# Optimization experiments

Hardware: AMD Instinct MI355X
Metric: run time of the kernel (lower is better)

## Reference

```python
import jax, jax.numpy as jnp
import numpy as np

B, T, D, H = 4, 4096, 256, 64  # batch, seq, DIM_EMBEDDING (fixed constant), head_size


def setup_inputs() -> dict:
    key = jax.random.key(0)
    ks = jax.random.split(key, 6)
    x = jax.random.normal(ks[0], (B, T, D), dtype=jnp.float32)
    scale = jnp.float32(0.02)
    Wq = jax.random.normal(ks[1], (D, H), dtype=jnp.float32) * scale
    Wk = jax.random.normal(ks[2], (D, H), dtype=jnp.float32) * scale
    Wv = jax.random.normal(ks[3], (D, H), dtype=jnp.float32) * scale
    two_pi = jnp.float32(2.0 * np.pi)
    angles_x = jax.random.uniform(ks[4], (T, H // 4), dtype=jnp.float32, maxval=two_pi)
    angles_y = jax.random.uniform(ks[5], (T, H // 4), dtype=jnp.float32, maxval=two_pi)
    return {"x": x, "Wq": Wq, "Wk": Wk, "Wv": Wv, "angles_x": angles_x, "angles_y": angles_y}


def _rope_half(v, freqs):
    # v: (B, T, H/2) real; freqs: (T, H/4) complex64 (unit phasors)
    b, t, h = v.shape
    vc = v.astype(jnp.float32).reshape(b, t, h // 2, 2)
    vz = jax.lax.complex(vc[..., 0], vc[..., 1])         # (B, T, H/4)
    rz = vz * freqs[None]                                 # complex multiply per position
    out = jnp.stack([jnp.real(rz), jnp.imag(rz)], axis=-1)
    return out.reshape(b, t, h)


def _rope2d(v, fx, fy):
    vx, vy = jnp.split(v, 2, axis=-1)
    return jnp.concatenate([_rope_half(vx, fx), _rope_half(vy, fy)], axis=-1)


def reference(x, Wq, Wk, Wv, angles_x, angles_y):
    # complex unit phasors e^{i*theta}
    fx = jax.lax.complex(jnp.cos(angles_x), jnp.sin(angles_x))
    fy = jax.lax.complex(jnp.cos(angles_y), jnp.sin(angles_y))
    # original apply_rotary_embeddings is wrapped in @torch.no_grad -> detached
    q = jax.lax.stop_gradient(_rope2d(x @ Wq, fx, fy))
    k = jax.lax.stop_gradient(_rope2d(x @ Wk, fx, fy))
    v = x @ Wv
    C = x.shape[-1]  # NOTE: source scales by embedding dim (256), not head dim
    wei = jnp.einsum('bth,bsh->bts', q, k) / jnp.sqrt(jnp.float32(C))
    softwei = jax.nn.softmax(wei, axis=-1)  # no causal mask in source
    out = jnp.einsum('bts,bsh->bth', softwei, v)
    return out
```

## Files before the change

### kernel.cpp

```cpp
#include <hip/hip_runtime.h>

#define B_ 4
#define T_ 4096
#define D_ 256
#define H_ 64
#define NBT (B_ * T_)
#define NBTH (B_ * T_ * H_)

typedef __bf16 bf16x8 __attribute__((ext_vector_type(8)));
typedef float f32x4 __attribute__((ext_vector_type(4)));

__device__ __forceinline__ unsigned short f2bf(float f) {
  union { float f; unsigned int u; } v; v.f = f;
  unsigned int u = v.u;
  return (unsigned short)((u + 0x7fffu + ((u >> 16) & 1u)) >> 16);
}

#if __has_builtin(__builtin_amdgcn_cvt_pk_bf16_f32)
typedef __bf16 bf16x2_t __attribute__((ext_vector_type(2)));
__device__ __forceinline__ unsigned int pk2(float a, float b) {
  union { bf16x2_t v; unsigned int u; } c;
  c.v = __builtin_amdgcn_cvt_pk_bf16_f32(a, b);
  return c.u;
}
#else
__device__ __forceinline__ unsigned int pk2(float a, float b) {
  return (unsigned int)f2bf(a) | ((unsigned int)f2bf(b) << 16);
}
#endif

#if __has_builtin(__builtin_amdgcn_exp2f)
#define EXP2(x) __builtin_amdgcn_exp2f(x)
#else
#define EXP2(x) exp2f(x)
#endif

#define QSCALE 0.09016844f


__global__ __launch_bounds__(256) void prep_w_kernel(
    const float* __restrict__ Wq, const float* __restrict__ Wk,
    const float* __restrict__ Wv, unsigned short* __restrict__ wt) {
  const int m = blockIdx.x;
  const float* W = (m == 0) ? Wq : (m == 1) ? Wk : Wv;
  const float scale = (m == 0) ? QSCALE : 1.f;
  __shared__ unsigned short tile[64][264];
  int h = threadIdx.x & 63, dq = threadIdx.x >> 6;
  for (int d = dq; d < D_; d += 4)
    tile[h][d] = f2bf(W[d * H_ + h] * scale);
  __syncthreads();
  int ht = threadIdx.x >> 6;
  int lane = threadIdx.x & 63, quad = lane >> 4, l16 = lane & 15;
#pragma unroll
  for (int c = 0; c < 8; ++c) {
    bf16x8 v = *(const bf16x8*)&tile[ht * 16 + l16][c * 32 + quad * 8];
    *(bf16x8*)&wt[(((m * 4 + ht) * 8 + c) << 9) + lane * 8] = v;
  }
}

__global__ __launch_bounds__(192) void qkv_kernel(
    const float* __restrict__ x, const unsigned short* __restrict__ wt,
    const float* __restrict__ axg, const float* __restrict__ ayg,
    unsigned short* __restrict__ qo, unsigned short* __restrict__ ko,
    unsigned short* __restrict__ vt) {
  const int row0g = blockIdx.x * 16;
  const int tid = threadIdx.x;
  const int w = tid / 64, lane = tid & 63, quad = lane >> 4, l16 = lane & 15;

  __shared__ unsigned short xs[16][264];
  __shared__ unsigned short qkt[2][16][72];
  __shared__ unsigned short vsh[64][16];

  const float4* xb = (const float4*)(x + (size_t)row0g * D_);
  for (int i = tid; i < 1024; i += 192) {
    float4 v = xb[i];
    int r = i >> 6, c4 = (i & 63) << 2;
    *(unsigned int*)&xs[r][c4] = pk2(v.x, v.y);
    *(unsigned int*)&xs[r][c4 + 2] = pk2(v.z, v.w);
  }
  __syncthreads();

  bf16x8 xf[8];
#pragma unroll
  for (int c = 0; c < 8; ++c)
    xf[c] = *(const bf16x8*)&xs[l16][c * 32 + quad * 8];

  const unsigned short* wb = wt + (((size_t)w * 4) * 8 << 9);
  f32x4 acc[4];
#pragma unroll
  for (int ht = 0; ht < 4; ++ht) acc[ht] = (f32x4){0.f, 0.f, 0.f, 0.f};
#pragma unroll
  for (int c = 0; c < 8; ++c) {
#pragma unroll
    for (int ht = 0; ht < 4; ++ht) {
      bf16x8 wf = *(const bf16x8*)&wb[((ht * 8 + c) << 9) + lane * 8];
      acc[ht] = __builtin_amdgcn_mfma_f32_16x16x32_bf16(xf[c], wf, acc[ht],
                                                        0, 0, 0);
    }
  }

  const int row0loc = row0g & (T_ - 1);
  if (w < 2) {
    const float sgn = (l16 & 1) ? 1.f : -1.f;
#pragma unroll
    for (int ht = 0; ht < 4; ++ht) {
      int hh = ht * 16 + l16;
      int pidx = (hh & 31) >> 1;
      const float* ab = (hh >= 32) ? ayg : axg;
#pragma unroll
      for (int r = 0; r < 4; ++r) {
        int t = row0loc + quad * 4 + r;
        float s, c;
        __sincosf(ab[t * 16 + pidx], &s, &c);
        float val = acc[ht][r];
        float par = __shfl_xor(val, 1);
        qkt[w][quad * 4 + r][hh] = f2bf(val * c + sgn * par * s);
      }
    }
    asm volatile("s_waitcnt lgkmcnt(0)" ::: "memory");
    unsigned short* dst;
    size_t base;
    if (w == 0) {
      dst = qo;
      base = ((size_t)(row0g >> 4) * 2) << 9;
    } else {
      dst = ko;
      base = ((size_t)((row0g >> 6) * 8 + ((row0g >> 4) & 3) * 2)) << 9;
    }
#pragma unroll
    for (int half = 0; half < 2; ++half) {
      bf16x8 v = *(const bf16x8*)&qkt[w][l16][half * 32 + quad * 8];
      *(bf16x8*)&dst[base + half * 512 + lane * 8] = v;
    }
  } else {
#pragma unroll
    for (int ht = 0; ht < 4; ++ht)
#pragma unroll
      for (int r = 0; r < 4; ++r)
        vsh[ht * 16 + l16][quad * 4 + r] = f2bf(acc[ht][r]);
    asm volatile("s_waitcnt lgkmcnt(0)" ::: "memory");
    const int kvblk = row0g >> 6;
    const int mt = (row0g >> 4) & 3;
    const int half_v = mt >> 1, qlow = (mt & 1) * 2;
#pragma unroll
    for (int it = 0; it < 2; ++it) {
      int hhx = it * 2 + (quad >> 1);
      int qp = qlow + (quad & 1);
      bf16x8 v = *(const bf16x8*)&vsh[hhx * 16 + l16][(quad & 1) * 8];
      *(bf16x8*)&vt[((((size_t)kvblk * 4 + hhx) * 2 + half_v) << 9) +
                    (qp * 16 + l16) * 8] = v;
    }
  }
}

#define LDP 72

__global__ __launch_bounds__(256, 3) void attn_kernel(
    const unsigned short* __restrict__ qfg, const unsigned short* __restrict__ kfg,
    const unsigned short* __restrict__ vfg, float* __restrict__ opart,
    float* __restrict__ lpart, int kv_len) {
  const int split = blockIdx.x >> 7;
  const int rem = blockIdx.x & 127;
  const int b = rem >> 5;
  const int q0 = (rem & 31) * 128;
  const int tid = threadIdx.x;
  const int w = tid >> 6, lane = tid & 63, quad = lane >> 4, l16 = lane & 15;

  __shared__ unsigned short Ps[4][32 * LDP];

  bf16x8 ones;
  {
    union { bf16x8 v; unsigned int u[4]; } c;
    c.u[0] = c.u[1] = c.u[2] = c.u[3] = 0x3F803F80u;
    ones = c.v;
  }

  bf16x8 qf[2][2];
#pragma unroll
  for (int u = 0; u < 2; ++u) {
    size_t rb = (size_t)(b * T_ + q0 + w * 32 + u * 16) >> 4;
#pragma unroll
    for (int half = 0; half < 2; ++half)
      qf[u][half] = *(const bf16x8*)&qfg[((rb * 2 + half) << 9) + lane * 8];
  }

  f32x4 oacc[2][4], lacc[2];
  const f32x4 vzero = {0.f, 0.f, 0.f, 0.f};
#pragma unroll
  for (int u = 0; u < 2; ++u) {
    lacc[u] = vzero;
#pragma unroll
    for (int hh = 0; hh < 4; ++hh) oacc[u][hh] = vzero;
  }

  const int kvb0 = (b * T_ + split * kv_len) >> 6;
  const int nkvb = kv_len >> 6;

  for (int kb = 0; kb < nkvb; ++kb) {
    const unsigned short* kfb = kfg + ((size_t)(kvb0 + kb) << 12);
    const unsigned short* vfb = vfg + ((size_t)(kvb0 + kb) << 12);

    f32x4 st[2][4];
#pragma unroll
    for (int mt = 0; mt < 4; ++mt) {
      bf16x8 k0 = *(const bf16x8*)&kfb[((mt * 2 + 0) << 9) + lane * 8];
      bf16x8 k1 = *(const bf16x8*)&kfb[((mt * 2 + 1) << 9) + lane * 8];
#pragma unroll
      for (int u = 0; u < 2; ++u) {
        f32x4 s = vzero;
        s = __builtin_amdgcn_mfma_f32_16x16x32_bf16(k0, qf[u][0], s, 0, 0, 0);
        s = __builtin_amdgcn_mfma_f32_16x16x32_bf16(k1, qf[u][1], s, 0, 0, 0);
        st[u][mt] = s;
      }
    }
#pragma unroll
    for (int u = 0; u < 2; ++u)
#pragma unroll
      for (int mt = 0; mt < 4; ++mt) {
        float p0 = EXP2(st[u][mt][0]);
        float p1 = EXP2(st[u][mt][1]);
        float p2 = EXP2(st[u][mt][2]);
        float p3 = EXP2(st[u][mt][3]);
        uint2 pk;
        pk.x = pk2(p0, p1);
        pk.y = pk2(p2, p3);
        *(uint2*)&Ps[w][(u * 16 + l16) * LDP + mt * 16 + quad * 4] = pk;
      }
    asm volatile("s_waitcnt lgkmcnt(0)" ::: "memory");

    bf16x8 ap[2][2];
#pragma unroll
    for (int u = 0; u < 2; ++u)
#pragma unroll
      for (int half = 0; half < 2; ++half)
        ap[u][half] =
            *(const bf16x8*)&Ps[w][(u * 16 + l16) * LDP + half * 32 + quad * 8];

#pragma unroll
    for (int hh = 0; hh < 4; ++hh) {
      bf16x8 v0 = *(const bf16x8*)&vfb[((hh * 2 + 0) << 9) + lane * 8];
      bf16x8 v1 = *(const bf16x8*)&vfb[((hh * 2 + 1) << 9) + lane * 8];
#pragma unroll
      for (int u = 0; u < 2; ++u) {
        oacc[u][hh] =
            __builtin_amdgcn_mfma_f32_16x16x32_bf16(ap[u][0], v0, oacc[u][hh], 0, 0, 0);
        oacc[u][hh] =
            __builtin_amdgcn_mfma_f32_16x16x32_bf16(ap[u][1], v1, oacc[u][hh], 0, 0, 0);
      }
    }
#pragma unroll
    for (int u = 0; u < 2; ++u) {
      lacc[u] = __builtin_amdgcn_mfma_f32_16x16x32_bf16(ap[u][0], ones, lacc[u], 0, 0, 0);
      lacc[u] = __builtin_amdgcn_mfma_f32_16x16x32_bf16(ap[u][1], ones, lacc[u], 0, 0, 0);
    }
  }

#pragma unroll
  for (int u = 0; u < 2; ++u) {
    size_t base = (size_t)(split * B_ + b) * T_ + q0 + w * 32 + u * 16;
#pragma unroll
    for (int r = 0; r < 4; ++r) {
      float* orow = opart + (base + quad * 4 + r) * H_;
#pragma unroll
      for (int hh = 0; hh < 4; ++hh) orow[hh * 16 + l16] = oacc[u][hh][r];
      if (l16 == 0) lpart[base + quad * 4 + r] = lacc[u][r];
    }
  }
}

__global__ __launch_bounds__(256) void combine_kernel(
    const float* __restrict__ opart, const float* __restrict__ lpart,
    float* __restrict__ out, int ns) {
  int idx = blockIdx.x * 256 + threadIdx.x;
  int bt = idx >> 4;
  float den = 0.f;
  float axx = 0.f, ayy = 0.f, azz = 0.f, aww = 0.f;
  for (int s = 0; s < ns; ++s) {
    den += lpart[s * NBT + bt];
    float4 o = ((const float4*)opart)[(size_t)s * (NBTH / 4) + idx];
    axx += o.x; ayy += o.y; azz += o.z; aww += o.w;
  }
  float inv = 1.f / den;
  float4 res;
  res.x = axx * inv; res.y = ayy * inv; res.z = azz * inv; res.w = aww * inv;
  ((float4*)out)[idx] = res;
}

extern "C" void kernel_launch(void* const* d_in, const int* in_sizes, int n_in,
                              void* d_out, int out_size, void* d_ws,
                              size_t ws_size, hipStream_t stream) {
  const float* x  = (const float*)d_in[0];
  const float* Wq = (const float*)d_in[1];
  const float* Wk = (const float*)d_in[2];
  const float* Wv = (const float*)d_in[3];
  const float* ax = (const float*)d_in[4];
  const float* ay = (const float*)d_in[5];
  float* out = (float*)d_out;

  unsigned short* qo = (unsigned short*)d_ws;
  unsigned short* ko = qo + NBTH;
  unsigned short* vt = ko + NBTH;
  unsigned short* wt = vt + NBTH;
  float* opart = (float*)(wt + 3 * H_ * D_);

  size_t fixed = (size_t)3 * NBTH * 2 + (size_t)3 * H_ * D_ * 2;
  int NS = (ws_size >= fixed + (size_t)8 * NBTH * 4 + (size_t)8 * NBT * 4 + 256)
               ? 8 : 4;
  float* lpart = opart + (size_t)NS * NBTH;

  prep_w_kernel<<<3, 256, 0, stream>>>(Wq, Wk, Wv, wt);
  qkv_kernel<<<NBT / 16, 192, 0, stream>>>(x, wt, ax, ay, qo, ko, vt);
  attn_kernel<<<NS * 128, 256, 0, stream>>>(qo, ko, vt, opart, lpart, T_ / NS);
  combine_kernel<<<NBTH / 4 / 256, 256, 0, stream>>>(opart, lpart, out, NS);
}
```

Baseline: 114.5 us.

## Raise attention occupancy, compute row sums on VALU, rotate KV block order

Launch bounds move from 3 to 4 waves-per-EU target. The softmax-denominator MFMAs against a ones vector are replaced by per-lane VALU sums reduced with cross-lane shuffles at the end. The exp is applied right after each score MFMA instead of via a staged score array, and P fragments are reloaded from LDS inside the PV loop, which cuts live registers. Each block also starts its KV loop at a rotated offset to spread concurrent blocks across memory. The trade-off is extra LDS reads per iteration and possible spilling under the tighter register cap.

```diff
diff --git a/kernel.cpp b/kernel.cpp
--- a/kernel.cpp
+++ b/kernel.cpp
@@ -155,7 +155,7 @@
 
 #define LDP 72
 
-__global__ __launch_bounds__(256, 3) void attn_kernel(
+__global__ __launch_bounds__(256, 4) void attn_kernel(
     const unsigned short* __restrict__ qfg, const unsigned short* __restrict__ kfg,
     const unsigned short* __restrict__ vfg, float* __restrict__ opart,
     float* __restrict__ lpart, int kv_len) {
@@ -168,13 +168,6 @@
 
   __shared__ unsigned short Ps[4][32 * LDP];
 
-  bf16x8 ones;
-  {
-    union { bf16x8 v; unsigned int u[4]; } c;
-    c.u[0] = c.u[1] = c.u[2] = c.u[3] = 0x3F803F80u;
-    ones = c.v;
-  }
-
   bf16x8 qf[2][2];
 #pragma unroll
   for (int u = 0; u < 2; ++u) {
@@ -184,23 +177,23 @@
       qf[u][half] = *(const bf16x8*)&qfg[((rb * 2 + half) << 9) + lane * 8];
   }
 
-  f32x4 oacc[2][4], lacc[2];
+  f32x4 oacc[2][4];
+  float lsum[2] = {0.f, 0.f};
   const f32x4 vzero = {0.f, 0.f, 0.f, 0.f};
 #pragma unroll
-  for (int u = 0; u < 2; ++u) {
-    lacc[u] = vzero;
+  for (int u = 0; u < 2; ++u)
 #pragma unroll
     for (int hh = 0; hh < 4; ++hh) oacc[u][hh] = vzero;
-  }
 
   const int kvb0 = (b * T_ + split * kv_len) >> 6;
   const int nkvb = kv_len >> 6;
-
-  for (int kb = 0; kb < nkvb; ++kb) {
+  const int rot = rem & (nkvb - 1);
+
+  for (int i = 0; i < nkvb; ++i) {
+    const int kb = (i + rot) & (nkvb - 1);
     const unsigned short* kfb = kfg + ((size_t)(kvb0 + kb) << 12);
     const unsigned short* vfb = vfg + ((size_t)(kvb0 + kb) << 12);
 
-    f32x4 st[2][4];
 #pragma unroll
     for (int mt = 0; mt < 4; ++mt) {
       bf16x8 k0 = *(const bf16x8*)&kfb[((mt * 2 + 0) << 9) + lane * 8];
@@ -210,31 +203,18 @@
         f32x4 s = vzero;
         s = __builtin_amdgcn_mfma_f32_16x16x32_bf16(k0, qf[u][0], s, 0, 0, 0);
         s = __builtin_amdgcn_mfma_f32_16x16x32_bf16(k1, qf[u][1], s, 0, 0, 0);
-        st[u][mt] = s;
-      }
-    }
-#pragma unroll
-    for (int u = 0; u < 2; ++u)
-#pragma unroll
-      for (int mt = 0; mt < 4; ++mt) {
-        float p0 = EXP2(st[u][mt][0]);
-        float p1 = EXP2(st[u][mt][1]);
-        float p2 = EXP2(st[u][mt][2]);
-        float p3 = EXP2(st[u][mt][3]);
+        float p0 = EXP2(s[0]);
+        float p1 = EXP2(s[1]);
+        float p2 = EXP2(s[2]);
+        float p3 = EXP2(s[3]);
+        lsum[u] += (p0 + p1) + (p2 + p3);
         uint2 pk;
         pk.x = pk2(p0, p1);
         pk.y = pk2(p2, p3);
         *(uint2*)&Ps[w][(u * 16 + l16) * LDP + mt * 16 + quad * 4] = pk;
       }
+    }
     asm volatile("s_waitcnt lgkmcnt(0)" ::: "memory");
-
-    bf16x8 ap[2][2];
-#pragma unroll
-    for (int u = 0; u < 2; ++u)
-#pragma unroll
-      for (int half = 0; half < 2; ++half)
-        ap[u][half] =
-            *(const bf16x8*)&Ps[w][(u * 16 + l16) * LDP + half * 32 + quad * 8];
 
 #pragma unroll
     for (int hh = 0; hh < 4; ++hh) {
@@ -242,28 +222,29 @@
       bf16x8 v1 = *(const bf16x8*)&vfb[((hh * 2 + 1) << 9) + lane * 8];
 #pragma unroll
       for (int u = 0; u < 2; ++u) {
+        bf16x8 ap0 =
+            *(const bf16x8*)&Ps[w][(u * 16 + l16) * LDP + quad * 8];
+        bf16x8 ap1 =
+            *(const bf16x8*)&Ps[w][(u * 16 + l16) * LDP + 32 + quad * 8];
         oacc[u][hh] =
-            __builtin_amdgcn_mfma_f32_16x16x32_bf16(ap[u][0], v0, oacc[u][hh], 0, 0, 0);
+            __builtin_amdgcn_mfma_f32_16x16x32_bf16(ap0, v0, oacc[u][hh], 0, 0, 0);
         oacc[u][hh] =
-            __builtin_amdgcn_mfma_f32_16x16x32_bf16(ap[u][1], v1, oacc[u][hh], 0, 0, 0);
+            __builtin_amdgcn_mfma_f32_16x16x32_bf16(ap1, v1, oacc[u][hh], 0, 0, 0);
       }
     }
-#pragma unroll
-    for (int u = 0; u < 2; ++u) {
-      lacc[u] = __builtin_amdgcn_mfma_f32_16x16x32_bf16(ap[u][0], ones, lacc[u], 0, 0, 0);
-      lacc[u] = __builtin_amdgcn_mfma_f32_16x16x32_bf16(ap[u][1], ones, lacc[u], 0, 0, 0);
-    }
   }
 
 #pragma unroll
   for (int u = 0; u < 2; ++u) {
+    lsum[u] += __shfl_xor(lsum[u], 16);
+    lsum[u] += __shfl_xor(lsum[u], 32);
     size_t base = (size_t)(split * B_ + b) * T_ + q0 + w * 32 + u * 16;
+    if (quad == 0) lpart[base + l16] = lsum[u];
 #pragma unroll
     for (int r = 0; r < 4; ++r) {
       float* orow = opart + (base + quad * 4 + r) * H_;
 #pragma unroll
       for (int hh = 0; hh < 4; ++hh) orow[hh * 16 + l16] = oacc[u][hh][r];
-      if (l16 == 0) lpart[base + quad * 4 + r] = lacc[u][r];
     }
   }
 }
```

Result: slower. 118.7 us (+3.7%).
